# Optimization experiments

Hardware: AMD Instinct MI355X
Metric: run time of the kernel (lower is better)

## Reference

```python
import jax, jax.numpy as jnp
import numpy as np

CONCORDANCE_EPSILON = 1e-8
RANKING_WEIGHT = 0.2
RANKING_SCALE = 1.0


def setup_inputs() -> dict:
    key = jax.random.key(0)
    k1, k2, k3 = jax.random.split(key, 3)
    N = 8192
    return {
        "risk_scores": jax.random.normal(k1, (N,), dtype=jnp.float32),
        "survival_times": jax.random.uniform(k2, (N,), dtype=jnp.float32),
        "event_indicators": jax.random.randint(k3, (N,), 0, 2, dtype=jnp.int32),
    }


def reference(risk_scores, survival_times, event_indicators):
    dtype = risk_scores.dtype
    # ---- likelihood term: negative partial log-likelihood over risk sets ----
    # Sort by survival time descending; risk set of i is the suffix [i:].
    order = jnp.argsort(-survival_times)
    r_sorted = risk_scores[order]
    e_sorted = event_indicators[order]
    # reverse cumulative logsumexp: rcls[i] = logsumexp(r_sorted[i:])
    rcls = jax.lax.cumlogsumexp(r_sorted, axis=0, reverse=True)
    n_events = jnp.sum(event_indicators).astype(dtype)
    likelihood = jnp.sum(jnp.where(e_sorted == 1, r_sorted - rcls, jnp.zeros((), dtype)))
    likelihood_loss = -likelihood / (n_events + CONCORDANCE_EPSILON)

    # ---- ranking term: for every ordered pair (a, b) with event_a == 1 and
    # t_a < t_b, accumulate exp(scale * (r_b - r_a)); average over pair count.
    # (The original i<j double loop with its elif covers exactly these pairs.)
    earlier = (event_indicators[:, None] == 1) & (
        survival_times[:, None] < survival_times[None, :]
    )  # [N, N] bool
    risk_diff = risk_scores[None, :] - risk_scores[:, None]  # r_b - r_a
    rank_sum = jnp.sum(jnp.where(earlier, jnp.exp(RANKING_SCALE * risk_diff), jnp.zeros((), dtype)))
    pair_count = jnp.sum(earlier).astype(dtype)
    ranking_loss = jnp.where(pair_count > 0, rank_sum / jnp.maximum(pair_count, 1.0), rank_sum)

    return likelihood_loss + RANKING_WEIGHT * ranking_loss
```

## Files before the change

### kernel.cpp

```cpp
#include <hip/hip_runtime.h>
#include <math.h>

#define NMAX 8192
#define TPB  512
#define APB  8


__global__ __launch_bounds__(TPB, 8)
void pair_scan(const float* __restrict__ t,
               const float* __restrict__ r,
               const int*   __restrict__ e,
               double* __restrict__ partials, int n) {
    __shared__ __align__(16) unsigned int sp[NMAX];
    __shared__ float  swx[8];
    __shared__ double red[8][4];

    const int tid  = threadIdx.x;
    const int lane = tid & 63;
    const int wid  = tid >> 6;

    float xsum = 0.f;
#pragma unroll
    for (int k = 0; k < NMAX / (TPB * 4); ++k) {
        const int li = tid * 4 + k * (TPB * 4);
        uint4 pw = make_uint4(0u, 0u, 0u, 0u);
        if (li + 3 < n) {
            const float4 tv = *(const float4*)(t + li);
            const float4 rv = *(const float4*)(r + li);
            const unsigned x0 = __float_as_uint(__expf(rv.x));
            const unsigned x1 = __float_as_uint(__expf(rv.y));
            const unsigned x2 = __float_as_uint(__expf(rv.z));
            const unsigned x3 = __float_as_uint(__expf(rv.w));
            pw.x = (__float_as_uint(tv.x) & 0xFFFF0000u) | ((x0 + 0x8000u) >> 16);
            pw.y = (__float_as_uint(tv.y) & 0xFFFF0000u) | ((x1 + 0x8000u) >> 16);
            pw.z = (__float_as_uint(tv.z) & 0xFFFF0000u) | ((x2 + 0x8000u) >> 16);
            pw.w = (__float_as_uint(tv.w) & 0xFFFF0000u) | ((x3 + 0x8000u) >> 16);
            xsum += __uint_as_float(pw.x << 16) + __uint_as_float(pw.y << 16)
                  + __uint_as_float(pw.z << 16) + __uint_as_float(pw.w << 16);
        } else {
#pragma unroll
            for (int m = 0; m < 4; ++m) {
                const int g = li + m;
                if (g < n) {
                    const unsigned xb = __float_as_uint(__expf(r[g]));
                    const unsigned w  = (__float_as_uint(t[g]) & 0xFFFF0000u) | ((xb + 0x8000u) >> 16);
                    ((unsigned*)&pw)[m] = w;
                    xsum += __uint_as_float(w << 16);
                }
            }
        }
        *(uint4*)(sp + li) = pw;
    }

    const int a   = blockIdx.x * APB + wid;
    const bool va = (a < n);
    const unsigned ka = va ? ((__float_as_uint(t[a]) & 0xFFFF0000u) | 0xFFFFu) : 0xFFFFFFFFu;
    const float ra    = va ? r[a] : 0.f;
    const int   ea    = va ? e[a] : 0;
    const bool  live  = va && (ea == 1);
    __syncthreads();

    float sgt = 0.f;
    int   cnt = 0;
    if (live) {
        uint4 c0 = *(const uint4*)(sp + lane * 4);
#pragma unroll 4
        for (int it = 0; it < 32; ++it) {
            uint4 nx = c0;
            if (it + 1 < 32) nx = *(const uint4*)(sp + (it + 1) * 256 + lane * 4);
            bool g;
            g = (c0.x > ka); sgt += g ? __uint_as_float(c0.x << 16) : 0.f; cnt += __popcll(__ballot(g));
            g = (c0.y > ka); sgt += g ? __uint_as_float(c0.y << 16) : 0.f; cnt += __popcll(__ballot(g));
            g = (c0.z > ka); sgt += g ? __uint_as_float(c0.z << 16) : 0.f; cnt += __popcll(__ballot(g));
            g = (c0.w > ka); sgt += g ? __uint_as_float(c0.w << 16) : 0.f; cnt += __popcll(__ballot(g));
            c0 = nx;
        }
    }

#pragma unroll
    for (int off = 32; off > 0; off >>= 1) {
        sgt  += __shfl_xor(sgt, off);
        xsum += __shfl_xor(xsum, off);
    }
    if (lane == 0) swx[wid] = xsum;
    __syncthreads();

    if (lane == 0) {
        float S = 0.f;
#pragma unroll
        for (int w = 0; w < 8; ++w) S += swx[w];
        double lik = 0.0, rnk = 0.0, pc = 0.0;
        if (live) {
            const float ssf = fmaxf(S - sgt, __expf(ra));
            lik = (double)(ra - __logf(ssf));
            rnk = (double)(sgt * __expf(-ra));
            pc  = (double)cnt;
        }
        red[wid][0] = lik; red[wid][1] = rnk; red[wid][2] = pc;
        red[wid][3] = live ? 1.0 : 0.0;
    }
    __syncthreads();
    if (tid == 0) {
        double lik = 0.0, rnk = 0.0, pc = 0.0, ev = 0.0;
#pragma unroll
        for (int w = 0; w < 8; ++w) {
            lik += red[w][0]; rnk += red[w][1]; pc += red[w][2]; ev += red[w][3];
        }
        partials[blockIdx.x * 4 + 0] = lik;
        partials[blockIdx.x * 4 + 1] = rnk;
        partials[blockIdx.x * 4 + 2] = pc;
        partials[blockIdx.x * 4 + 3] = ev;
    }
}

__global__ __launch_bounds__(256)
void finalize_kernel(const double* __restrict__ partials,
                     int nblocks, float* __restrict__ out) {
    __shared__ double sl[256], sr[256], sc[256], se[256];
    const int tid = threadIdx.x;
    double lik = 0.0, rnk = 0.0, pc = 0.0, ev = 0.0;
    for (int i = tid; i < nblocks; i += 256) {
        lik += partials[i * 4 + 0];
        rnk += partials[i * 4 + 1];
        pc  += partials[i * 4 + 2];
        ev  += partials[i * 4 + 3];
    }
    sl[tid] = lik; sr[tid] = rnk; sc[tid] = pc; se[tid] = ev;
    __syncthreads();
    for (int s = 128; s > 0; s >>= 1) {
        if (tid < s) {
            sl[tid] += sl[tid + s]; sr[tid] += sr[tid + s];
            sc[tid] += sc[tid + s]; se[tid] += se[tid + s];
        }
        __syncthreads();
    }
    if (tid == 0) {
        const float nev  = (float)se[0];
        const float likf = (float)sl[0];
        const float rnkf = (float)sr[0];
        const float pcf  = (float)sc[0];
        const float likelihood_loss = -likf / (nev + 1e-8f);
        const float ranking_loss = (pcf > 0.f) ? (rnkf / fmaxf(pcf, 1.f)) : rnkf;
        out[0] = likelihood_loss + 0.2f * ranking_loss;
    }
}

extern "C" void kernel_launch(void* const* d_in, const int* in_sizes, int n_in,
                              void* d_out, int out_size, void* d_ws, size_t ws_size,
                              hipStream_t stream) {
    const float* risk   = (const float*)d_in[0];
    const float* times  = (const float*)d_in[1];
    const int*   events = (const int*)d_in[2];
    float* out = (float*)d_out;
    const int n = in_sizes[0];

    double* partials = (double*)d_ws;
    const int nblocks = (n + APB - 1) / APB;

    pair_scan<<<nblocks, TPB, 0, stream>>>(times, risk, events, partials, n);
    finalize_kernel<<<1, 256, 0, stream>>>(partials, nblocks, out);
}
```

Before: 19.27 us.

## Precompute packed time/exp-risk words once and fuse finalize via last-block reduction

Adds a small pre-pass kernel that computes the packed (time-high-bits | bf16 exp(risk)) words once into workspace, so each of the 1024 scan blocks only copies them into shared memory instead of recomputing 8192 exps. The separate finalize kernel is removed: each block bumps a global atomic counter after writing its partials, and the last block does the final reduction, reusing shared memory. This trades one kernel launch for another and adds a global-memory round trip plus atomic and fence overhead per block.

```diff
diff --git a/kernel.cpp b/kernel.cpp
--- a/kernel.cpp
+++ b/kernel.cpp
@@ -5,15 +5,33 @@
 #define TPB  512
 #define APB  8
 
+__device__ int g_counter = 0;
+
+__global__ __launch_bounds__(512)
+void pack_kernel(const float* __restrict__ t,
+                 const float* __restrict__ r,
+                 unsigned int* __restrict__ packed, int n) {
+    const int i = blockIdx.x * 512 + threadIdx.x;
+    if (i >= NMAX) return;
+    unsigned w = 0u;
+    if (i < n) {
+        const unsigned xb = __float_as_uint(__expf(r[i]));
+        w = (__float_as_uint(t[i]) & 0xFFFF0000u) | ((xb + 0x8000u) >> 16);
+    }
+    packed[i] = w;
+}
 
 __global__ __launch_bounds__(TPB, 8)
 void pair_scan(const float* __restrict__ t,
                const float* __restrict__ r,
                const int*   __restrict__ e,
-               double* __restrict__ partials, int n) {
+               const unsigned int* __restrict__ packed,
+               double* __restrict__ partials,
+               float* __restrict__ out, int n, int nblocks) {
     __shared__ __align__(16) unsigned int sp[NMAX];
     __shared__ float  swx[8];
     __shared__ double red[8][4];
+    __shared__ int    slast;
 
     const int tid  = threadIdx.x;
     const int lane = tid & 63;
@@ -23,33 +41,10 @@
 #pragma unroll
     for (int k = 0; k < NMAX / (TPB * 4); ++k) {
         const int li = tid * 4 + k * (TPB * 4);
-        uint4 pw = make_uint4(0u, 0u, 0u, 0u);
-        if (li + 3 < n) {
-            const float4 tv = *(const float4*)(t + li);
-            const float4 rv = *(const float4*)(r + li);
-            const unsigned x0 = __float_as_uint(__expf(rv.x));
-            const unsigned x1 = __float_as_uint(__expf(rv.y));
-            const unsigned x2 = __float_as_uint(__expf(rv.z));
-            const unsigned x3 = __float_as_uint(__expf(rv.w));
-            pw.x = (__float_as_uint(tv.x) & 0xFFFF0000u) | ((x0 + 0x8000u) >> 16);
-            pw.y = (__float_as_uint(tv.y) & 0xFFFF0000u) | ((x1 + 0x8000u) >> 16);
-            pw.z = (__float_as_uint(tv.z) & 0xFFFF0000u) | ((x2 + 0x8000u) >> 16);
-            pw.w = (__float_as_uint(tv.w) & 0xFFFF0000u) | ((x3 + 0x8000u) >> 16);
-            xsum += __uint_as_float(pw.x << 16) + __uint_as_float(pw.y << 16)
-                  + __uint_as_float(pw.z << 16) + __uint_as_float(pw.w << 16);
-        } else {
-#pragma unroll
-            for (int m = 0; m < 4; ++m) {
-                const int g = li + m;
-                if (g < n) {
-                    const unsigned xb = __float_as_uint(__expf(r[g]));
-                    const unsigned w  = (__float_as_uint(t[g]) & 0xFFFF0000u) | ((xb + 0x8000u) >> 16);
-                    ((unsigned*)&pw)[m] = w;
-                    xsum += __uint_as_float(w << 16);
-                }
-            }
-        }
+        const uint4 pw = *(const uint4*)(packed + li);
         *(uint4*)(sp + li) = pw;
+        xsum += __uint_as_float(pw.x << 16) + __uint_as_float(pw.y << 16)
+              + __uint_as_float(pw.z << 16) + __uint_as_float(pw.w << 16);
     }
 
     const int a   = blockIdx.x * APB + wid;
@@ -110,38 +105,46 @@
         partials[blockIdx.x * 4 + 1] = rnk;
         partials[blockIdx.x * 4 + 2] = pc;
         partials[blockIdx.x * 4 + 3] = ev;
+        __threadfence();
+        const int old = atomicAdd(&g_counter, 1);
+        slast = (old == nblocks - 1) ? 1 : 0;
+        if (slast) g_counter = 0;
     }
-}
+    __syncthreads();
 
-__global__ __launch_bounds__(256)
-void finalize_kernel(const double* __restrict__ partials,
-                     int nblocks, float* __restrict__ out) {
-    __shared__ double sl[256], sr[256], sc[256], se[256];
-    const int tid = threadIdx.x;
-    double lik = 0.0, rnk = 0.0, pc = 0.0, ev = 0.0;
-    for (int i = tid; i < nblocks; i += 256) {
-        lik += partials[i * 4 + 0];
-        rnk += partials[i * 4 + 1];
-        pc  += partials[i * 4 + 2];
-        ev  += partials[i * 4 + 3];
-    }
-    sl[tid] = lik; sr[tid] = rnk; sc[tid] = pc; se[tid] = ev;
-    __syncthreads();
-    for (int s = 128; s > 0; s >>= 1) {
-        if (tid < s) {
-            sl[tid] += sl[tid + s]; sr[tid] += sr[tid + s];
-            sc[tid] += sc[tid + s]; se[tid] += se[tid + s];
+    if (slast) {
+        __threadfence();
+        double lik = 0.0, rnk = 0.0, pc = 0.0, ev = 0.0;
+        for (int i = tid; i < nblocks; i += TPB) {
+            lik += partials[i * 4 + 0];
+            rnk += partials[i * 4 + 1];
+            pc  += partials[i * 4 + 2];
+            ev  += partials[i * 4 + 3];
         }
+        double* dl = (double*)sp;
+        dl[tid]         = lik;
+        dl[512 + tid]   = rnk;
+        dl[1024 + tid]  = pc;
+        dl[1536 + tid]  = ev;
         __syncthreads();
-    }
-    if (tid == 0) {
-        const float nev  = (float)se[0];
-        const float likf = (float)sl[0];
-        const float rnkf = (float)sr[0];
-        const float pcf  = (float)sc[0];
-        const float likelihood_loss = -likf / (nev + 1e-8f);
-        const float ranking_loss = (pcf > 0.f) ? (rnkf / fmaxf(pcf, 1.f)) : rnkf;
-        out[0] = likelihood_loss + 0.2f * ranking_loss;
+        for (int s = 256; s > 0; s >>= 1) {
+            if (tid < s) {
+                dl[tid]        += dl[tid + s];
+                dl[512 + tid]  += dl[512 + tid + s];
+                dl[1024 + tid] += dl[1024 + tid + s];
+                dl[1536 + tid] += dl[1536 + tid + s];
+            }
+            __syncthreads();
+        }
+        if (tid == 0) {
+            const float nev  = (float)dl[1536];
+            const float likf = (float)dl[0];
+            const float rnkf = (float)dl[512];
+            const float pcf  = (float)dl[1024];
+            const float likelihood_loss = -likf / (nev + 1e-8f);
+            const float ranking_loss = (pcf > 0.f) ? (rnkf / fmaxf(pcf, 1.f)) : rnkf;
+            out[0] = likelihood_loss + 0.2f * ranking_loss;
+        }
     }
 }
 
@@ -154,9 +157,11 @@
     float* out = (float*)d_out;
     const int n = in_sizes[0];
 
-    double* partials = (double*)d_ws;
+    unsigned int* packed   = (unsigned int*)d_ws;
+    double*       partials = (double*)((char*)d_ws + NMAX * sizeof(unsigned));
     const int nblocks = (n + APB - 1) / APB;
 
-    pair_scan<<<nblocks, TPB, 0, stream>>>(times, risk, events, partials, n);
-    finalize_kernel<<<1, 256, 0, stream>>>(partials, nblocks, out);
+    pack_kernel<<<NMAX / 512, 512, 0, stream>>>(times, risk, packed, n);
+    pair_scan<<<nblocks, TPB, 0, stream>>>(times, risk, events, packed,
+                                           partials, out, n, nblocks);
 }
```

Result: slower. 38.13 us (+97.9%).

## Process two anchors per wave and more anchors per block to amortize staging

Applied to the files above, without the earlier changes.

Blocks grow from 512 to 1024 threads, and each wavefront now scores two anchor samples against the shared packed time/exp(risk) table instead of one. Each block therefore covers 32 anchors instead of 8. This cuts the number of blocks that each redundantly rebuild the 8192-entry LDS table, and reuses every LDS load for two comparisons. The finalize kernel is reduced to a single wavefront using shuffle reductions instead of a shared-memory tree. In exchange there is more register pressure, fewer blocks for latency hiding, and wasted work in waves where only one of the two anchors is an event.

```diff
diff --git a/kernel.cpp b/kernel.cpp
--- a/kernel.cpp
+++ b/kernel.cpp
@@ -2,18 +2,18 @@
 #include <math.h>
 
 #define NMAX 8192
-#define TPB  512
-#define APB  8
+#define TPB  1024
+#define APB  32
 
 
-__global__ __launch_bounds__(TPB, 8)
+__global__ __launch_bounds__(TPB, 4)
 void pair_scan(const float* __restrict__ t,
                const float* __restrict__ r,
                const int*   __restrict__ e,
                double* __restrict__ partials, int n) {
     __shared__ __align__(16) unsigned int sp[NMAX];
-    __shared__ float  swx[8];
-    __shared__ double red[8][4];
+    __shared__ float  swx[16];
+    __shared__ double red[16][4];
 
     const int tid  = threadIdx.x;
     const int lane = tid & 63;
@@ -52,34 +52,46 @@
         *(uint4*)(sp + li) = pw;
     }
 
-    const int a   = blockIdx.x * APB + wid;
-    const bool va = (a < n);
-    const unsigned ka = va ? ((__float_as_uint(t[a]) & 0xFFFF0000u) | 0xFFFFu) : 0xFFFFFFFFu;
-    const float ra    = va ? r[a] : 0.f;
-    const int   ea    = va ? e[a] : 0;
-    const bool  live  = va && (ea == 1);
+    const int a0 = blockIdx.x * APB + wid * 2;
+    const int a1 = a0 + 1;
+    const bool v0 = (a0 < n), v1 = (a1 < n);
+    const unsigned ka0 = v0 ? ((__float_as_uint(t[a0]) & 0xFFFF0000u) | 0xFFFFu) : 0xFFFFFFFFu;
+    const unsigned ka1 = v1 ? ((__float_as_uint(t[a1]) & 0xFFFF0000u) | 0xFFFFu) : 0xFFFFFFFFu;
+    const float ra0 = v0 ? r[a0] : 0.f;
+    const float ra1 = v1 ? r[a1] : 0.f;
+    const int   ea0 = v0 ? e[a0] : 0;
+    const int   ea1 = v1 ? e[a1] : 0;
+    const bool  live = (v0 && ea0 == 1) || (v1 && ea1 == 1);
     __syncthreads();
 
-    float sgt = 0.f;
-    int   cnt = 0;
+    float sg0 = 0.f, sg1 = 0.f;
+    int   cn0 = 0,   cn1 = 0;
     if (live) {
         uint4 c0 = *(const uint4*)(sp + lane * 4);
 #pragma unroll 4
         for (int it = 0; it < 32; ++it) {
             uint4 nx = c0;
             if (it + 1 < 32) nx = *(const uint4*)(sp + (it + 1) * 256 + lane * 4);
-            bool g;
-            g = (c0.x > ka); sgt += g ? __uint_as_float(c0.x << 16) : 0.f; cnt += __popcll(__ballot(g));
-            g = (c0.y > ka); sgt += g ? __uint_as_float(c0.y << 16) : 0.f; cnt += __popcll(__ballot(g));
-            g = (c0.z > ka); sgt += g ? __uint_as_float(c0.z << 16) : 0.f; cnt += __popcll(__ballot(g));
-            g = (c0.w > ka); sgt += g ? __uint_as_float(c0.w << 16) : 0.f; cnt += __popcll(__ballot(g));
+            {   const unsigned w = c0.x; const float xv = __uint_as_float(w << 16);
+                const bool g0 = w > ka0; sg0 += g0 ? xv : 0.f; cn0 += __popcll(__ballot(g0));
+                const bool g1 = w > ka1; sg1 += g1 ? xv : 0.f; cn1 += __popcll(__ballot(g1)); }
+            {   const unsigned w = c0.y; const float xv = __uint_as_float(w << 16);
+                const bool g0 = w > ka0; sg0 += g0 ? xv : 0.f; cn0 += __popcll(__ballot(g0));
+                const bool g1 = w > ka1; sg1 += g1 ? xv : 0.f; cn1 += __popcll(__ballot(g1)); }
+            {   const unsigned w = c0.z; const float xv = __uint_as_float(w << 16);
+                const bool g0 = w > ka0; sg0 += g0 ? xv : 0.f; cn0 += __popcll(__ballot(g0));
+                const bool g1 = w > ka1; sg1 += g1 ? xv : 0.f; cn1 += __popcll(__ballot(g1)); }
+            {   const unsigned w = c0.w; const float xv = __uint_as_float(w << 16);
+                const bool g0 = w > ka0; sg0 += g0 ? xv : 0.f; cn0 += __popcll(__ballot(g0));
+                const bool g1 = w > ka1; sg1 += g1 ? xv : 0.f; cn1 += __popcll(__ballot(g1)); }
             c0 = nx;
         }
     }
 
 #pragma unroll
     for (int off = 32; off > 0; off >>= 1) {
-        sgt  += __shfl_xor(sgt, off);
+        sg0  += __shfl_xor(sg0, off);
+        sg1  += __shfl_xor(sg1, off);
         xsum += __shfl_xor(xsum, off);
     }
     if (lane == 0) swx[wid] = xsum;
@@ -88,22 +100,29 @@
     if (lane == 0) {
         float S = 0.f;
 #pragma unroll
-        for (int w = 0; w < 8; ++w) S += swx[w];
-        double lik = 0.0, rnk = 0.0, pc = 0.0;
-        if (live) {
-            const float ssf = fmaxf(S - sgt, __expf(ra));
-            lik = (double)(ra - __logf(ssf));
-            rnk = (double)(sgt * __expf(-ra));
-            pc  = (double)cnt;
+        for (int w = 0; w < 16; ++w) S += swx[w];
+        double lik = 0.0, rnk = 0.0, pc = 0.0, ev = 0.0;
+        if (v0 && ea0 == 1) {
+            const float ssf = fmaxf(S - sg0, __expf(ra0));
+            lik += (double)(ra0 - __logf(ssf));
+            rnk += (double)(sg0 * __expf(-ra0));
+            pc  += (double)cn0;
+            ev  += 1.0;
         }
-        red[wid][0] = lik; red[wid][1] = rnk; red[wid][2] = pc;
-        red[wid][3] = live ? 1.0 : 0.0;
+        if (v1 && ea1 == 1) {
+            const float ssf = fmaxf(S - sg1, __expf(ra1));
+            lik += (double)(ra1 - __logf(ssf));
+            rnk += (double)(sg1 * __expf(-ra1));
+            pc  += (double)cn1;
+            ev  += 1.0;
+        }
+        red[wid][0] = lik; red[wid][1] = rnk; red[wid][2] = pc; red[wid][3] = ev;
     }
     __syncthreads();
     if (tid == 0) {
         double lik = 0.0, rnk = 0.0, pc = 0.0, ev = 0.0;
 #pragma unroll
-        for (int w = 0; w < 8; ++w) {
+        for (int w = 0; w < 16; ++w) {
             lik += red[w][0]; rnk += red[w][1]; pc += red[w][2]; ev += red[w][3];
         }
         partials[blockIdx.x * 4 + 0] = lik;
@@ -113,32 +132,29 @@
     }
 }
 
-__global__ __launch_bounds__(256)
+__global__ __launch_bounds__(64)
 void finalize_kernel(const double* __restrict__ partials,
                      int nblocks, float* __restrict__ out) {
-    __shared__ double sl[256], sr[256], sc[256], se[256];
-    const int tid = threadIdx.x;
+    const int lane = threadIdx.x;
     double lik = 0.0, rnk = 0.0, pc = 0.0, ev = 0.0;
-    for (int i = tid; i < nblocks; i += 256) {
+    for (int i = lane; i < nblocks; i += 64) {
         lik += partials[i * 4 + 0];
         rnk += partials[i * 4 + 1];
         pc  += partials[i * 4 + 2];
         ev  += partials[i * 4 + 3];
     }
-    sl[tid] = lik; sr[tid] = rnk; sc[tid] = pc; se[tid] = ev;
-    __syncthreads();
-    for (int s = 128; s > 0; s >>= 1) {
-        if (tid < s) {
-            sl[tid] += sl[tid + s]; sr[tid] += sr[tid + s];
-            sc[tid] += sc[tid + s]; se[tid] += se[tid + s];
-        }
-        __syncthreads();
+#pragma unroll
+    for (int off = 32; off > 0; off >>= 1) {
+        lik += __shfl_xor(lik, off);
+        rnk += __shfl_xor(rnk, off);
+        pc  += __shfl_xor(pc,  off);
+        ev  += __shfl_xor(ev,  off);
     }
-    if (tid == 0) {
-        const float nev  = (float)se[0];
-        const float likf = (float)sl[0];
-        const float rnkf = (float)sr[0];
-        const float pcf  = (float)sc[0];
+    if (lane == 0) {
+        const float nev  = (float)ev;
+        const float likf = (float)lik;
+        const float rnkf = (float)rnk;
+        const float pcf  = (float)pc;
         const float likelihood_loss = -likf / (nev + 1e-8f);
         const float ranking_loss = (pcf > 0.f) ? (rnkf / fmaxf(pcf, 1.f)) : rnkf;
         out[0] = likelihood_loss + 0.2f * ranking_loss;
@@ -158,5 +174,5 @@
     const int nblocks = (n + APB - 1) / APB;
 
     pair_scan<<<nblocks, TPB, 0, stream>>>(times, risk, events, partials, n);
-    finalize_kernel<<<1, 256, 0, stream>>>(partials, nblocks, out);
+    finalize_kernel<<<1, 64, 0, stream>>>(partials, nblocks, out);
 }
```

After: 17.44 us. 9.5% less time.
